# Performance work log

Measured on AMD Instinct MI355X. Metric: run time of the kernel, lower is better.

## Reference

```python
import jax, jax.numpy as jnp
import numpy as np
import math

D_MODEL = 1024
NUM_HEADS = 16
HEAD_DIM = D_MODEL // NUM_HEADS
BLOCK_SIZE = 64
THRESHOLD = 0.99


def setup_inputs() -> dict:
    key = jax.random.key(0)
    ks = jax.random.split(key, 12)
    B, S, D = 2, 2048, D_MODEL
    scale = 1.0 / math.sqrt(D)
    x = jax.random.normal(ks[0], (B, S, D), dtype=jnp.float32)
    G_ii = jax.random.uniform(ks[1], (B, S), dtype=jnp.float32)
    # Linear weights stored as [in, out]; applied as x @ W + b (matches nn.Linear math).
    Wq = jax.random.normal(ks[2], (D, D), dtype=jnp.float32) * scale
    bq = jnp.zeros((D,), dtype=jnp.float32)
    Wk = jax.random.normal(ks[3], (D, D), dtype=jnp.float32) * scale
    bk = jnp.zeros((D,), dtype=jnp.float32)
    Wv = jax.random.normal(ks[4], (D, D), dtype=jnp.float32) * scale
    bv = jnp.zeros((D,), dtype=jnp.float32)
    Wo = jax.random.normal(ks[5], (D, D), dtype=jnp.float32) * scale
    bo = jnp.zeros((D,), dtype=jnp.float32)
    return {"x": x, "G_ii": G_ii, "Wq": Wq, "bq": bq, "Wk": Wk, "bk": bk,
            "Wv": Wv, "bv": bv, "Wo": Wo, "bo": bo}


def reference(x, G_ii, Wq, bq, Wk, bk, Wv, bv, Wo, bo):
    B, S, D = x.shape
    H, hd, bs = NUM_HEADS, HEAD_DIM, BLOCK_SIZE
    nb = S // bs

    # Projections and head split: [B, H, S, hd]
    q = (x @ Wq + bq).reshape(B, S, H, hd).transpose(0, 2, 1, 3)
    k = (x @ Wk + bk).reshape(B, S, H, hd).transpose(0, 2, 1, 3)
    v = (x @ Wv + bv).reshape(B, S, H, hd).transpose(0, 2, 1, 3)

    # Per-query-block scattering energy keep mask: block kept iff max |G_ii| >= threshold
    energy = jnp.abs(G_ii)                              # [B, S]
    block_max = energy.reshape(B, nb, bs).max(axis=-1)  # [B, nb]
    keep = (block_max >= THRESHOLD)                     # [B, nb] bool
    row_keep = jnp.repeat(keep, bs, axis=1)             # [B, S]

    # Kept query blocks attend densely (non-causal) over all keys; skipped blocks output zero.
    scores = jnp.einsum('bhqd,bhkd->bhqk', q, k) / math.sqrt(hd)  # [B, H, S, S]
    attn = jax.nn.softmax(scores, axis=-1)
    out = jnp.einsum('bhqk,bhkd->bhqd', attn, v)                  # [B, H, S, hd]
    out = out * row_keep[:, None, :, None].astype(out.dtype)

    out = out.transpose(0, 2, 1, 3).reshape(B, S, D)
    return out @ Wo + bo
```

## Files before the change

kernel.cpp:

```cpp
#include <hip/hip_runtime.h>
#include <math.h>

#define D_MODEL   1024
#define NUM_HEADS 16
#define HEAD_DIM  64
#define BS        64
#define NB        32
#define S_LEN     2048
#define BATCH     2
#define M_ROWS    (BATCH * S_LEN)
#define THRESH    0.99f
#define SCEXP     0.18033688f
#define NPH       (BATCH * NB * NUM_HEADS)
#define SPLITK    4

typedef __attribute__((ext_vector_type(8))) short bf16x8;
typedef __attribute__((ext_vector_type(8))) _Float16 f16x8;
typedef __attribute__((ext_vector_type(2))) __fp16 fp16v2;
typedef __attribute__((ext_vector_type(4))) float f32x4;

static constexpr size_t QKV_ELEMS = (size_t)BATCH * NUM_HEADS * S_LEN * HEAD_DIM;

__device__ __forceinline__ unsigned short f2bf(float f) {
    unsigned int u = __float_as_uint(f);
    u += 0x7fff + ((u >> 16) & 1);
    return (unsigned short)(u >> 16);
}

__device__ __forceinline__ unsigned int pkrtz(float a, float b) {
    fp16v2 r = __builtin_amdgcn_cvt_pkrtz(a, b);
    return __builtin_bit_cast(unsigned int, r);
}

__device__ __forceinline__ void gload16(const void* gptr, void* lptr) {
    __builtin_amdgcn_global_load_lds(
        (const __attribute__((address_space(1))) void*)gptr,
        (__attribute__((address_space(3))) void*)lptr, 16, 0, 0);
}

__global__ __launch_bounds__(256) void prep_kernel(
    const float* __restrict__ x, const float* __restrict__ G,
    const float* __restrict__ Wq, const float* __restrict__ Wk,
    const float* __restrict__ Wv, const float* __restrict__ Wo,
    unsigned short* __restrict__ xb, unsigned short* __restrict__ wcat,
    unsigned short* __restrict__ wot, int* __restrict__ keep, int* __restrict__ work)
{
    const int bid = blockIdx.x, tid = threadIdx.x;
    __shared__ float T[64][65];

    if (bid < 2048) {
        size_t i = ((size_t)bid * 256 + tid) * 8;
        float4 a = *(const float4*)(x + i);
        float4 b = *(const float4*)(x + i + 4);
        uint4 o;
        o.x = (unsigned int)f2bf(a.x) | ((unsigned int)f2bf(a.y) << 16);
        o.y = (unsigned int)f2bf(a.z) | ((unsigned int)f2bf(a.w) << 16);
        o.z = (unsigned int)f2bf(b.x) | ((unsigned int)f2bf(b.y) << 16);
        o.w = (unsigned int)f2bf(b.z) | ((unsigned int)f2bf(b.w) << 16);
        *(uint4*)(xb + i) = o;
    } else if (bid < 3072) {
        int i = bid - 2048;
        int mat = i >> 8, rem = i & 255;
        int k0 = (rem & 15) * 64, n0 = (rem >> 4) * 64;
        const float* W = (mat == 0) ? Wq : (mat == 1) ? Wk : (mat == 2) ? Wv : Wo;
        int rr = tid >> 4, c4 = (tid & 15) * 4;
        #pragma unroll
        for (int j = 0; j < 4; j++) {
            int row = rr + j * 16;
            float4 v = *(const float4*)(W + (size_t)(k0 + row) * 1024 + n0 + c4);
            T[row][c4 + 0] = v.x; T[row][c4 + 1] = v.y;
            T[row][c4 + 2] = v.z; T[row][c4 + 3] = v.w;
        }
        __syncthreads();
        unsigned short* dst = (mat < 3) ? (wcat + (size_t)mat * 1024 * 1024) : wot;
        #pragma unroll
        for (int j = 0; j < 4; j++) {
            int n = rr + j * 16;
            unsigned int lo = (unsigned int)f2bf(T[c4 + 0][n]) | ((unsigned int)f2bf(T[c4 + 1][n]) << 16);
            unsigned int hi = (unsigned int)f2bf(T[c4 + 2][n]) | ((unsigned int)f2bf(T[c4 + 3][n]) << 16);
            *(uint2*)(dst + (size_t)(n0 + n) * 1024 + k0 + c4) = make_uint2(lo, hi);
        }
    } else {
        if (tid < 64) {
            int t = tid;
            const float4* g = (const float4*)(G + (size_t)t * 64);
            float mx = 0.f;
            #pragma unroll
            for (int j = 0; j < 16; j++) {
                float4 v = g[j];
                mx = fmaxf(mx, fmaxf(fmaxf(fabsf(v.x), fabsf(v.y)), fmaxf(fabsf(v.z), fabsf(v.w))));
            }
            bool k = (mx >= THRESH);
            unsigned long long bal = __ballot(k);
            int nk = __popcll(bal);
            unsigned long long below = bal & ((1ull << t) - 1ull);
            int nbelow = (int)__popcll(below);
            keep[t] = k ? 1 : 0;
            if (t == 0) work[0] = nk;
            int pos = k ? nbelow : (nk + t - nbelow);
            work[1 + pos] = t;
        }
    }
}

__global__ __launch_bounds__(256) void mfma_gemm(
    const unsigned short* __restrict__ A, const unsigned short* __restrict__ Bt,
    const float* __restrict__ b0, const float* __restrict__ b1, const float* __restrict__ b2,
    const int* __restrict__ keep,
    void* __restrict__ out0, unsigned short* __restrict__ out1, unsigned short* __restrict__ out2,
    int mode)
{
    const int K = 1024;
    const int n0 = blockIdx.x * 128, m0 = blockIdx.y * 128;
    const int tid = threadIdx.x, w = tid >> 6, lane = tid & 63;
    const int quad = lane >> 4, l16 = lane & 15;
    const int wm = w >> 1, wn = w & 1;

    const int kb0 = m0 >> 6;
    const bool dropped = (!keep[kb0]) && (!keep[kb0 + 1]);

    if (mode == 1 && (n0 >> 10) == 0 && dropped) return;
    if (mode == 0 && dropped) {
        float* o = (float*)out0;
        #pragma unroll
        for (int i = 0; i < 16; i++) {
            int u = tid + i * 256;
            int row = u >> 5, c = (u & 31) * 4;
            *(float4*)(o + (size_t)(m0 + row) * 1024 + n0 + c) = *(const float4*)(b0 + n0 + c);
        }
        return;
    }

    __shared__ unsigned short Asl[2][128 * 32];
    __shared__ unsigned short Bsl[2][128 * 32];

    f32x4 acc[4][4];
    #pragma unroll
    for (int mt = 0; mt < 4; mt++)
        #pragma unroll
        for (int nt = 0; nt < 4; nt++) acc[mt][nt] = (f32x4){0.f, 0.f, 0.f, 0.f};

    #define GSTAGE(it_, p_)                                                             \
        {                                                                               \
            int k0_ = (it_) * 32;                                                       \
            _Pragma("unroll")                                                           \
            for (int j = 0; j < 2; j++) {                                               \
                int s = w * 128 + j * 64 + lane;                                        \
                int row = s >> 2, cl = s & 3;                                           \
                int c = cl ^ ((row >> 1) & 3);                                          \
                gload16(A  + (size_t)(m0 + row) * K + k0_ + c * 8,                      \
                        &Asl[p_][(size_t)(w * 128 + j * 64) * 8]);                      \
                gload16(Bt + (size_t)(n0 + row) * K + k0_ + c * 8,                      \
                        &Bsl[p_][(size_t)(w * 128 + j * 64) * 8]);                      \
            }                                                                           \
        }

    GSTAGE(0, 0)

    for (int it = 0; it < 32; it++) {
        const int p = it & 1;
        __syncthreads();
        if (it + 1 < 32) GSTAGE(it + 1, (it + 1) & 1)

        bf16x8 af[4], bfr[4];
        #pragma unroll
        for (int mt = 0; mt < 4; mt++) {
            int row = wm * 64 + mt * 16 + l16;
            int cl = quad ^ ((row >> 1) & 3);
            af[mt] = *(const bf16x8*)&Asl[p][(row * 4 + cl) * 8];
        }
        #pragma unroll
        for (int nt = 0; nt < 4; nt++) {
            int row = wn * 64 + nt * 16 + l16;
            int cl = quad ^ ((row >> 1) & 3);
            bfr[nt] = *(const bf16x8*)&Bsl[p][(row * 4 + cl) * 8];
        }
        #pragma unroll
        for (int mt = 0; mt < 4; mt++)
            #pragma unroll
            for (int nt = 0; nt < 4; nt++)
                acc[mt][nt] = __builtin_amdgcn_mfma_f32_16x16x32_bf16(af[mt], bfr[nt], acc[mt][nt], 0, 0, 0);
    }

    if (mode == 0) {
        float* o = (float*)out0;
        #pragma unroll
        for (int nt = 0; nt < 4; nt++) {
            int col = n0 + wn * 64 + nt * 16 + l16;
            float bb = b0[col];
            #pragma unroll
            for (int mt = 0; mt < 4; mt++) {
                int mb = m0 + wm * 64 + mt * 16 + quad * 4;
                #pragma unroll
                for (int r = 0; r < 4; r++)
                    o[(size_t)(mb + r) * 1024 + col] = acc[mt][nt][r] + bb;
            }
        }
    } else {
        #pragma unroll
        for (int nt = 0; nt < 4; nt++) {
            int col = n0 + wn * 64 + nt * 16 + l16;
            int kind = col >> 10, cc = col & 1023;
            int h = cc >> 6, d = cc & 63;
            const float* bp = (kind == 0) ? b0 : (kind == 1) ? b1 : b2;
            float bb = bp[cc];
            #pragma unroll
            for (int mt = 0; mt < 4; mt++) {
                int m = m0 + wm * 64 + mt * 16 + quad * 4;
                int b = m >> 11, s = m & 2047;
                if (kind < 2) {
                    unsigned short* dst = ((kind == 0) ? (unsigned short*)out0 : out1) +
                        ((size_t)(b * NUM_HEADS + h) * S_LEN + s) * HEAD_DIM + d;
                    float sc = (kind == 0) ? SCEXP : 1.0f;
                    #pragma unroll
                    for (int r = 0; r < 4; r++)
                        dst[(size_t)r * HEAD_DIM] = f2bf((acc[mt][nt][r] + bb) * sc);
                } else {
                    unsigned int lo = pkrtz(acc[mt][nt][0] + bb, acc[mt][nt][1] + bb);
                    unsigned int hi = pkrtz(acc[mt][nt][2] + bb, acc[mt][nt][3] + bb);
                    *(uint2*)(out2 + ((size_t)(b * NUM_HEADS + h) * HEAD_DIM + d) * S_LEN + s) =
                        make_uint2(lo, hi);
                }
            }
        }
    }
}

__global__ __launch_bounds__(256, 4) void attn_kernel(
    const unsigned short* __restrict__ Q, const unsigned short* __restrict__ K,
    const unsigned short* __restrict__ Vtg, const int* __restrict__ work,
    unsigned short* __restrict__ opart, float* __restrict__ lpart)
{
    const int bx = blockIdx.x, half = blockIdx.y;
    const int pair = bx >> 4, h = bx & 15;
    const int tid  = threadIdx.x;
    const int w    = tid >> 6, lane = tid & 63;
    const int quad = lane >> 4, l16 = lane & 15;

    if (pair >= work[0]) return;
    const int e = work[1 + pair];
    const int b = e >> 5, qblk = e & 31;

    __shared__ unsigned short Kbuf[BS * HEAD_DIM];
    __shared__ unsigned short Vbuf[HEAD_DIM * BS];
    __shared__ unsigned short Pt[4][16 * 64];

    const int KEYS = S_LEN / SPLITK;
    const int NCH  = KEYS / BS;
    const size_t bh = (size_t)(b * NUM_HEADS + h);
    const unsigned short* Kb = K + bh * S_LEN * HEAD_DIM + (size_t)half * KEYS * HEAD_DIM;
    const unsigned short* Vb = Vtg + bh * HEAD_DIM * S_LEN + (size_t)half * KEYS;
    const unsigned short* Qb = Q + bh * S_LEN * HEAD_DIM;

    const int qrow = qblk * BS + w * 16 + l16;
    bf16x8 qf[2];
    #pragma unroll
    for (int ks = 0; ks < 2; ks++)
        qf[ks] = *(const bf16x8*)(Qb + (size_t)qrow * HEAD_DIM + ks * 32 + quad * 8);

    f32x4 o[4];
    #pragma unroll
    for (int mt = 0; mt < 4; mt++) o[mt] = (f32x4){0.f, 0.f, 0.f, 0.f};
    float l = 0.f;

    const int sA = w * 128 + lane, sB = sA + 64;
    const int rA = sA >> 3, cA = (sA & 7) ^ (rA & 7);
    const int rB = sB >> 3, cB = (sB & 7) ^ (rB & 7);
    const size_t koA = (size_t)rA * HEAD_DIM + cA * 8, koB = (size_t)rB * HEAD_DIM + cB * 8;
    const size_t voA = (size_t)rA * S_LEN + cA * 8,    voB = (size_t)rB * S_LEN + cB * 8;

    uint4 kr0, kr1, vr0, vr1;
    #define LOADREGS(kc_)                                                       \
        {                                                                       \
            const unsigned short* kg_ = Kb + (size_t)(kc_) * BS * HEAD_DIM;     \
            const unsigned short* vg_ = Vb + (size_t)(kc_) * BS;                \
            kr0 = *(const uint4*)(kg_ + koA); kr1 = *(const uint4*)(kg_ + koB); \
            vr0 = *(const uint4*)(vg_ + voA); vr1 = *(const uint4*)(vg_ + voB); \
        }
    #define WRITELDS()                                                          \
        {                                                                       \
            *(uint4*)&Kbuf[(size_t)sA * 8] = kr0;                               \
            *(uint4*)&Kbuf[(size_t)sB * 8] = kr1;                               \
            *(uint4*)&Vbuf[(size_t)sA * 8] = vr0;                               \
            *(uint4*)&Vbuf[(size_t)sB * 8] = vr1;                               \
        }

    LOADREGS(0)
    WRITELDS()
    __syncthreads();

    for (int kc = 0; kc < NCH; kc++) {
        if (kc + 1 < NCH) LOADREGS(kc + 1)

        f32x4 st[4];
        #pragma unroll
        for (int mt = 0; mt < 4; mt++) {
            f32x4 acc = {0.f, 0.f, 0.f, 0.f};
            #pragma unroll
            for (int ks = 0; ks < 2; ks++) {
                int kk = mt * 16 + l16;
                bf16x8 kf = *(const bf16x8*)&Kbuf[(size_t)(kk * 8 + ((ks * 4 + quad) ^ (kk & 7))) * 8];
                acc = __builtin_amdgcn_mfma_f32_16x16x32_bf16(kf, qf[ks], acc, 0, 0, 0);
            }
            st[mt] = acc;
        }

        float pv[16], sum = 0.f;
        #pragma unroll
        for (int mt = 0; mt < 4; mt++)
            #pragma unroll
            for (int r = 0; r < 4; r++) {
                float ex = exp2f(st[mt][r]);
                pv[mt * 4 + r] = ex; sum += ex;
            }
        sum += __shfl_xor(sum, 16, 64);
        sum += __shfl_xor(sum, 32, 64);
        l += sum;

        #pragma unroll
        for (int mt = 0; mt < 4; mt++) {
            unsigned int lo = pkrtz(pv[mt * 4 + 0], pv[mt * 4 + 1]);
            unsigned int hi = pkrtz(pv[mt * 4 + 2], pv[mt * 4 + 3]);
            int c16 = 2 * mt + (quad >> 1);
            *(uint2*)&Pt[w][l16 * 64 + ((c16 ^ (l16 & 7)) * 8 + (quad & 1) * 4)] = make_uint2(lo, hi);
        }

        #pragma unroll
        for (int ks = 0; ks < 2; ks++) {
            f16x8 pf = *(const f16x8*)&Pt[w][l16 * 64 + (((4 * ks + quad) ^ (l16 & 7)) * 8)];
            #pragma unroll
            for (int mt = 0; mt < 4; mt++) {
                int d = mt * 16 + l16;
                f16x8 vf = *(const f16x8*)&Vbuf[(size_t)(d * 8 + ((ks * 4 + quad) ^ (d & 7))) * 8];
                o[mt] = __builtin_amdgcn_mfma_f32_16x16x32_f16(vf, pf, o[mt], 0, 0, 0);
            }
        }

        __syncthreads();
        if (kc + 1 < NCH) {
            WRITELDS()
            __syncthreads();
        }
    }

    unsigned short* ob = opart + ((size_t)(half * NPH + bx)) * 4096 + tid * 16;
    uint4 w0, w1;
    w0.x = pkrtz(o[0][0], o[0][1]); w0.y = pkrtz(o[0][2], o[0][3]);
    w0.z = pkrtz(o[1][0], o[1][1]); w0.w = pkrtz(o[1][2], o[1][3]);
    w1.x = pkrtz(o[2][0], o[2][1]); w1.y = pkrtz(o[2][2], o[2][3]);
    w1.z = pkrtz(o[3][0], o[3][1]); w1.w = pkrtz(o[3][2], o[3][3]);
    *(uint4*)ob = w0;
    *(uint4*)(ob + 8) = w1;
    if (quad == 0) lpart[(size_t)(half * NPH + bx) * 64 + w * 16 + l16] = l;
}

__global__ __launch_bounds__(256) void attn_combine(
    const unsigned short* __restrict__ opart, const float* __restrict__ lpart,
    const int* __restrict__ work, unsigned short* __restrict__ attn_out)
{
    const int bx = blockIdx.x;
    const int pair = bx >> 4, h = bx & 15;
    const int tid  = threadIdx.x;
    const int w    = tid >> 6, lane = tid & 63;
    const int quad = lane >> 4, l16 = lane & 15;

    const int e = work[1 + pair];
    const int b = e >> 5, qblk = e & 31;
    unsigned short* ablk = attn_out + ((size_t)(b * S_LEN + qblk * BS)) * D_MODEL + h * HEAD_DIM;

    if (pair >= work[0]) {
        uint4 z = make_uint4(0, 0, 0, 0);
        #pragma unroll
        for (int i = 0; i < 2; i++) {
            int u = tid + i * 256;
            int row = u >> 3, c8 = (u & 7) * 8;
            *(uint4*)(ablk + (size_t)row * D_MODEL + c8) = z;
        }
        return;
    }

    __shared__ float Obuf[4][HEAD_DIM * 17];

    float osum[16];
    #pragma unroll
    for (int j = 0; j < 16; j++) osum[j] = 0.f;
    float lsum = 0.f;
    #pragma unroll
    for (int hf = 0; hf < SPLITK; hf++) {
        const f16x8* pp = (const f16x8*)(opart + ((size_t)hf * NPH + bx) * 4096 + tid * 16);
        f16x8 a0 = pp[0], a1 = pp[1];
        #pragma unroll
        for (int j = 0; j < 8; j++) {
            osum[j]     += (float)a0[j];
            osum[8 + j] += (float)a1[j];
        }
        lsum += lpart[((size_t)hf * NPH + bx) * 64 + w * 16 + l16];
    }
    float inv = 1.0f / lsum;

    #pragma unroll
    for (int mt = 0; mt < 4; mt++)
        #pragma unroll
        for (int r = 0; r < 4; r++)
            Obuf[w][(mt * 16 + quad * 4 + r) * 17 + l16] = osum[mt * 4 + r] * inv;
    #pragma unroll
    for (int i = 0; i < 4; i++) {
        int uu = lane + 64 * i;
        int row = uu >> 4, d4 = (uu & 15) * 4;
        float x0 = Obuf[w][(d4 + 0) * 17 + row];
        float x1 = Obuf[w][(d4 + 1) * 17 + row];
        float x2 = Obuf[w][(d4 + 2) * 17 + row];
        float x3 = Obuf[w][(d4 + 3) * 17 + row];
        unsigned int lo = (unsigned int)f2bf(x0) | ((unsigned int)f2bf(x1) << 16);
        unsigned int hi = (unsigned int)f2bf(x2) | ((unsigned int)f2bf(x3) << 16);
        *(uint2*)(ablk + (size_t)(w * 16 + row) * D_MODEL + d4) = make_uint2(lo, hi);
    }
}

extern "C" void kernel_launch(void* const* d_in, const int* in_sizes, int n_in,
                              void* d_out, int out_size, void* d_ws, size_t ws_size,
                              hipStream_t stream) {
    const float* x  = (const float*)d_in[0];
    const float* G  = (const float*)d_in[1];
    const float* Wq = (const float*)d_in[2];
    const float* bq = (const float*)d_in[3];
    const float* Wk = (const float*)d_in[4];
    const float* bk = (const float*)d_in[5];
    const float* Wv = (const float*)d_in[6];
    const float* bv = (const float*)d_in[7];
    const float* Wo = (const float*)d_in[8];
    const float* bo = (const float*)d_in[9];
    float* out = (float*)d_out;

    char* wsp = (char*)d_ws;
    int* keep = (int*)wsp;
    int* work = keep + 64;
    unsigned short* xb    = (unsigned short*)(wsp + 1024);
    unsigned short* wcat  = xb + (size_t)M_ROWS * D_MODEL;
    unsigned short* wot   = wcat + (size_t)3 * 1024 * 1024;
    unsigned short* q     = wot + (size_t)1024 * 1024;
    unsigned short* k     = q + QKV_ELEMS;
    unsigned short* vt    = k + QKV_ELEMS;
    unsigned short* attnb = vt + QKV_ELEMS;
    unsigned short* opart = attnb + (size_t)M_ROWS * D_MODEL;
    float* lpart = (float*)(opart + (size_t)SPLITK * NPH * 4096);

    prep_kernel<<<3073, 256, 0, stream>>>(x, G, Wq, Wk, Wv, Wo, xb, wcat, wot, keep, work);

    mfma_gemm<<<dim3(3072 / 128, M_ROWS / 128), 256, 0, stream>>>(
        xb, wcat, bq, bk, bv, keep, (void*)q, k, vt, 1);

    attn_kernel<<<dim3(NPH, SPLITK), 256, 0, stream>>>(q, k, vt, work, opart, lpart);
    attn_combine<<<NPH, 256, 0, stream>>>(opart, lpart, work, attnb);

    mfma_gemm<<<dim3(1024 / 128, M_ROWS / 128), 256, 0, stream>>>(
        attnb, wot, bo, nullptr, nullptr, keep, (void*)out, nullptr, nullptr, 0);
}
```

Baseline: 197.5 us.

## Split GEMM into QKV and output kernels with smaller tiles and coalesced LDS epilogues

Replaces the unified 128x128 GEMM with two specialized kernels. gemm_qkv uses 64x128 tiles, skips Q at single 64-row block granularity, and stages results through LDS to write Q/K row-major into a combined [M,2048] buffer and V transposed with 16-byte stores. gemm_out uses 64x64 tiles with per-block keep skipping. The attention kernel reads Q/K from the new strided layout. Smaller tiles raise the block count and skip granularity but lower per-block data reuse.

```diff
diff --git a/kernel.cpp b/kernel.cpp
--- a/kernel.cpp
+++ b/kernel.cpp
@@ -18,8 +18,6 @@
 typedef __attribute__((ext_vector_type(8))) _Float16 f16x8;
 typedef __attribute__((ext_vector_type(2))) __fp16 fp16v2;
 typedef __attribute__((ext_vector_type(4))) float f32x4;
-
-static constexpr size_t QKV_ELEMS = (size_t)BATCH * NUM_HEADS * S_LEN * HEAD_DIM;
 
 __device__ __forceinline__ unsigned short f2bf(float f) {
     unsigned int u = __float_as_uint(f);
@@ -103,132 +101,205 @@
     }
 }
 
-__global__ __launch_bounds__(256) void mfma_gemm(
+__global__ __launch_bounds__(256, 4) void gemm_qkv(
     const unsigned short* __restrict__ A, const unsigned short* __restrict__ Bt,
-    const float* __restrict__ b0, const float* __restrict__ b1, const float* __restrict__ b2,
-    const int* __restrict__ keep,
-    void* __restrict__ out0, unsigned short* __restrict__ out1, unsigned short* __restrict__ out2,
-    int mode)
+    const float* __restrict__ bq, const float* __restrict__ bk, const float* __restrict__ bv,
+    const int* __restrict__ keep, unsigned short* __restrict__ qk, unsigned short* __restrict__ vt)
 {
-    const int K = 1024;
-    const int n0 = blockIdx.x * 128, m0 = blockIdx.y * 128;
+    const int n0 = blockIdx.x * 128, m0 = blockIdx.y * 64;
+    const int tid = threadIdx.x, w = tid >> 6, lane = tid & 63;
+    const int quad = lane >> 4, l16 = lane & 15;
+    const int kindb = n0 >> 10;
+    if (kindb == 0 && !keep[blockIdx.y]) return;
+
+    __shared__ union {
+        struct { unsigned short As[2][64 * 32]; unsigned short Bs[2][128 * 32]; } s;
+        unsigned short qkr[64 * 136];
+        unsigned short vr[128 * 72];
+    } u;
+
+    f32x4 acc[4][2];
+    #pragma unroll
+    for (int mt = 0; mt < 4; mt++)
+        #pragma unroll
+        for (int nt = 0; nt < 2; nt++) acc[mt][nt] = (f32x4){0.f, 0.f, 0.f, 0.f};
+
+    #define QSTAGE(it_, p_)                                                             \
+        {                                                                               \
+            int k0_ = (it_) * 32;                                                       \
+            { int s_ = w * 64 + lane; int row = s_ >> 2, cl = s_ & 3;                   \
+              int c = cl ^ ((row >> 1) & 3);                                            \
+              gload16(A + (size_t)(m0 + row) * 1024 + k0_ + c * 8,                      \
+                      &u.s.As[p_][(w * 64) * 8]); }                                     \
+            _Pragma("unroll")                                                           \
+            for (int j = 0; j < 2; j++) {                                               \
+                int s_ = w * 128 + j * 64 + lane; int row = s_ >> 2, cl = s_ & 3;       \
+                int c = cl ^ ((row >> 1) & 3);                                          \
+                gload16(Bt + (size_t)(n0 + row) * 1024 + k0_ + c * 8,                   \
+                        &u.s.Bs[p_][(w * 128 + j * 64) * 8]);                           \
+            }                                                                           \
+        }
+
+    QSTAGE(0, 0)
+
+    for (int it = 0; it < 32; it++) {
+        const int p = it & 1;
+        __syncthreads();
+        if (it + 1 < 32) QSTAGE(it + 1, (it + 1) & 1)
+
+        bf16x8 af[4], bfr[2];
+        #pragma unroll
+        for (int mt = 0; mt < 4; mt++) {
+            int row = mt * 16 + l16;
+            int cl = quad ^ ((row >> 1) & 3);
+            af[mt] = *(const bf16x8*)&u.s.As[p][(row * 4 + cl) * 8];
+        }
+        #pragma unroll
+        for (int nt = 0; nt < 2; nt++) {
+            int row = w * 32 + nt * 16 + l16;
+            int cl = quad ^ ((row >> 1) & 3);
+            bfr[nt] = *(const bf16x8*)&u.s.Bs[p][(row * 4 + cl) * 8];
+        }
+        #pragma unroll
+        for (int mt = 0; mt < 4; mt++)
+            #pragma unroll
+            for (int nt = 0; nt < 2; nt++)
+                acc[mt][nt] = __builtin_amdgcn_mfma_f32_16x16x32_bf16(af[mt], bfr[nt], acc[mt][nt], 0, 0, 0);
+    }
+    __syncthreads();
+
+    if (kindb < 2) {
+        const float* bp = (kindb == 0) ? bq : bk;
+        const float sc = (kindb == 0) ? SCEXP : 1.0f;
+        #pragma unroll
+        for (int nt = 0; nt < 2; nt++) {
+            int coll = w * 32 + nt * 16 + l16;
+            float bb = bp[(n0 & 1023) + coll];
+            #pragma unroll
+            for (int mt = 0; mt < 4; mt++)
+                #pragma unroll
+                for (int r = 0; r < 4; r++) {
+                    int row = mt * 16 + quad * 4 + r;
+                    u.qkr[row * 136 + coll] = f2bf((acc[mt][nt][r] + bb) * sc);
+                }
+        }
+        __syncthreads();
+        #pragma unroll
+        for (int i = 0; i < 4; i++) {
+            int s_ = tid + i * 256;
+            int row = s_ >> 4, c16 = s_ & 15;
+            uint4 v = *(const uint4*)&u.qkr[row * 136 + c16 * 8];
+            *(uint4*)(qk + (size_t)(m0 + row) * 2048 + n0 + c16 * 8) = v;
+        }
+    } else {
+        #pragma unroll
+        for (int nt = 0; nt < 2; nt++) {
+            int coll = w * 32 + nt * 16 + l16;
+            float bb = bv[(n0 - 2048) + coll];
+            #pragma unroll
+            for (int mt = 0; mt < 4; mt++) {
+                int s0 = mt * 16 + quad * 4;
+                uint2 pv;
+                pv.x = pkrtz(acc[mt][nt][0] + bb, acc[mt][nt][1] + bb);
+                pv.y = pkrtz(acc[mt][nt][2] + bb, acc[mt][nt][3] + bb);
+                *(uint2*)&u.vr[coll * 72 + s0] = pv;
+            }
+        }
+        __syncthreads();
+        const int b_ = m0 >> 11, sbase = m0 & 2047;
+        #pragma unroll
+        for (int i = 0; i < 4; i++) {
+            int s_ = tid + i * 256;
+            int coll = s_ >> 3, ch = s_ & 7;
+            uint4 v = *(const uint4*)&u.vr[coll * 72 + ch * 8];
+            int colg = n0 - 2048 + coll;
+            int h_ = colg >> 6, d = colg & 63;
+            *(uint4*)(vt + ((size_t)(b_ * NUM_HEADS + h_) * HEAD_DIM + d) * 2048 + sbase + ch * 8) = v;
+        }
+    }
+}
+
+__global__ __launch_bounds__(256, 4) void gemm_out(
+    const unsigned short* __restrict__ A, const unsigned short* __restrict__ Bt,
+    const float* __restrict__ bo, const int* __restrict__ keep, float* __restrict__ out)
+{
+    const int n0 = blockIdx.x * 64, m0 = blockIdx.y * 64;
     const int tid = threadIdx.x, w = tid >> 6, lane = tid & 63;
     const int quad = lane >> 4, l16 = lane & 15;
     const int wm = w >> 1, wn = w & 1;
 
-    const int kb0 = m0 >> 6;
-    const bool dropped = (!keep[kb0]) && (!keep[kb0 + 1]);
-
-    if (mode == 1 && (n0 >> 10) == 0 && dropped) return;
-    if (mode == 0 && dropped) {
-        float* o = (float*)out0;
-        #pragma unroll
-        for (int i = 0; i < 16; i++) {
-            int u = tid + i * 256;
-            int row = u >> 5, c = (u & 31) * 4;
-            *(float4*)(o + (size_t)(m0 + row) * 1024 + n0 + c) = *(const float4*)(b0 + n0 + c);
+    if (!keep[blockIdx.y]) {
+        #pragma unroll
+        for (int i = 0; i < 4; i++) {
+            int s_ = tid + i * 256;
+            int row = s_ >> 4, c = (s_ & 15) * 4;
+            *(float4*)(out + (size_t)(m0 + row) * 1024 + n0 + c) = *(const float4*)(bo + n0 + c);
         }
         return;
     }
 
-    __shared__ unsigned short Asl[2][128 * 32];
-    __shared__ unsigned short Bsl[2][128 * 32];
-
-    f32x4 acc[4][4];
-    #pragma unroll
-    for (int mt = 0; mt < 4; mt++)
-        #pragma unroll
-        for (int nt = 0; nt < 4; nt++) acc[mt][nt] = (f32x4){0.f, 0.f, 0.f, 0.f};
-
-    #define GSTAGE(it_, p_)                                                             \
+    __shared__ unsigned short Asl[2][64 * 32];
+    __shared__ unsigned short Bsl[2][64 * 32];
+
+    f32x4 acc[2][2];
+    #pragma unroll
+    for (int mt = 0; mt < 2; mt++)
+        #pragma unroll
+        for (int nt = 0; nt < 2; nt++) acc[mt][nt] = (f32x4){0.f, 0.f, 0.f, 0.f};
+
+    #define OSTAGE(it_, p_)                                                             \
         {                                                                               \
             int k0_ = (it_) * 32;                                                       \
-            _Pragma("unroll")                                                           \
-            for (int j = 0; j < 2; j++) {                                               \
-                int s = w * 128 + j * 64 + lane;                                        \
-                int row = s >> 2, cl = s & 3;                                           \
-                int c = cl ^ ((row >> 1) & 3);                                          \
-                gload16(A  + (size_t)(m0 + row) * K + k0_ + c * 8,                      \
-                        &Asl[p_][(size_t)(w * 128 + j * 64) * 8]);                      \
-                gload16(Bt + (size_t)(n0 + row) * K + k0_ + c * 8,                      \
-                        &Bsl[p_][(size_t)(w * 128 + j * 64) * 8]);                      \
-            }                                                                           \
-        }
-
-    GSTAGE(0, 0)
+            int s_ = w * 64 + lane; int row = s_ >> 2, cl = s_ & 3;                     \
+            int c = cl ^ ((row >> 1) & 3);                                              \
+            gload16(A  + (size_t)(m0 + row) * 1024 + k0_ + c * 8, &Asl[p_][(w * 64) * 8]); \
+            gload16(Bt + (size_t)(n0 + row) * 1024 + k0_ + c * 8, &Bsl[p_][(w * 64) * 8]); \
+        }
+
+    OSTAGE(0, 0)
 
     for (int it = 0; it < 32; it++) {
         const int p = it & 1;
         __syncthreads();
-        if (it + 1 < 32) GSTAGE(it + 1, (it + 1) & 1)
-
-        bf16x8 af[4], bfr[4];
-        #pragma unroll
-        for (int mt = 0; mt < 4; mt++) {
-            int row = wm * 64 + mt * 16 + l16;
+        if (it + 1 < 32) OSTAGE(it + 1, (it + 1) & 1)
+
+        bf16x8 af[2], bfr[2];
+        #pragma unroll
+        for (int mt = 0; mt < 2; mt++) {
+            int row = wm * 32 + mt * 16 + l16;
             int cl = quad ^ ((row >> 1) & 3);
             af[mt] = *(const bf16x8*)&Asl[p][(row * 4 + cl) * 8];
         }
         #pragma unroll
-        for (int nt = 0; nt < 4; nt++) {
-            int row = wn * 64 + nt * 16 + l16;
+        for (int nt = 0; nt < 2; nt++) {
+            int row = wn * 32 + nt * 16 + l16;
             int cl = quad ^ ((row >> 1) & 3);
             bfr[nt] = *(const bf16x8*)&Bsl[p][(row * 4 + cl) * 8];
         }
         #pragma unroll
-        for (int mt = 0; mt < 4; mt++)
-            #pragma unroll
-            for (int nt = 0; nt < 4; nt++)
+        for (int mt = 0; mt < 2; mt++)
+            #pragma unroll
+            for (int nt = 0; nt < 2; nt++)
                 acc[mt][nt] = __builtin_amdgcn_mfma_f32_16x16x32_bf16(af[mt], bfr[nt], acc[mt][nt], 0, 0, 0);
     }
 
-    if (mode == 0) {
-        float* o = (float*)out0;
-        #pragma unroll
-        for (int nt = 0; nt < 4; nt++) {
-            int col = n0 + wn * 64 + nt * 16 + l16;
-            float bb = b0[col];
-            #pragma unroll
-            for (int mt = 0; mt < 4; mt++) {
-                int mb = m0 + wm * 64 + mt * 16 + quad * 4;
-                #pragma unroll
-                for (int r = 0; r < 4; r++)
-                    o[(size_t)(mb + r) * 1024 + col] = acc[mt][nt][r] + bb;
-            }
-        }
-    } else {
-        #pragma unroll
-        for (int nt = 0; nt < 4; nt++) {
-            int col = n0 + wn * 64 + nt * 16 + l16;
-            int kind = col >> 10, cc = col & 1023;
-            int h = cc >> 6, d = cc & 63;
-            const float* bp = (kind == 0) ? b0 : (kind == 1) ? b1 : b2;
-            float bb = bp[cc];
-            #pragma unroll
-            for (int mt = 0; mt < 4; mt++) {
-                int m = m0 + wm * 64 + mt * 16 + quad * 4;
-                int b = m >> 11, s = m & 2047;
-                if (kind < 2) {
-                    unsigned short* dst = ((kind == 0) ? (unsigned short*)out0 : out1) +
-                        ((size_t)(b * NUM_HEADS + h) * S_LEN + s) * HEAD_DIM + d;
-                    float sc = (kind == 0) ? SCEXP : 1.0f;
-                    #pragma unroll
-                    for (int r = 0; r < 4; r++)
-                        dst[(size_t)r * HEAD_DIM] = f2bf((acc[mt][nt][r] + bb) * sc);
-                } else {
-                    unsigned int lo = pkrtz(acc[mt][nt][0] + bb, acc[mt][nt][1] + bb);
-                    unsigned int hi = pkrtz(acc[mt][nt][2] + bb, acc[mt][nt][3] + bb);
-                    *(uint2*)(out2 + ((size_t)(b * NUM_HEADS + h) * HEAD_DIM + d) * S_LEN + s) =
-                        make_uint2(lo, hi);
-                }
-            }
+    #pragma unroll
+    for (int nt = 0; nt < 2; nt++) {
+        int col = n0 + wn * 32 + nt * 16 + l16;
+        float bb = bo[col];
+        #pragma unroll
+        for (int mt = 0; mt < 2; mt++) {
+            int mb = m0 + wm * 32 + mt * 16 + quad * 4;
+            #pragma unroll
+            for (int r = 0; r < 4; r++)
+                out[(size_t)(mb + r) * 1024 + col] = acc[mt][nt][r] + bb;
         }
     }
 }
 
 __global__ __launch_bounds__(256, 4) void attn_kernel(
-    const unsigned short* __restrict__ Q, const unsigned short* __restrict__ K,
-    const unsigned short* __restrict__ Vtg, const int* __restrict__ work,
+    const unsigned short* __restrict__ qk, const unsigned short* __restrict__ Vtg,
+    const int* __restrict__ work,
     unsigned short* __restrict__ opart, float* __restrict__ lpart)
 {
     const int bx = blockIdx.x, half = blockIdx.y;
@@ -247,16 +318,15 @@
 
     const int KEYS = S_LEN / SPLITK;
     const int NCH  = KEYS / BS;
-    const size_t bh = (size_t)(b * NUM_HEADS + h);
-    const unsigned short* Kb = K + bh * S_LEN * HEAD_DIM + (size_t)half * KEYS * HEAD_DIM;
-    const unsigned short* Vb = Vtg + bh * HEAD_DIM * S_LEN + (size_t)half * KEYS;
-    const unsigned short* Qb = Q + bh * S_LEN * HEAD_DIM;
+    const unsigned short* Qb = qk + (size_t)(b * S_LEN) * 2048 + h * 64;
+    const unsigned short* Kb = qk + (size_t)(b * S_LEN + half * KEYS) * 2048 + 1024 + h * 64;
+    const unsigned short* Vb = Vtg + (size_t)(b * NUM_HEADS + h) * HEAD_DIM * 2048 + half * KEYS;
 
     const int qrow = qblk * BS + w * 16 + l16;
     bf16x8 qf[2];
     #pragma unroll
     for (int ks = 0; ks < 2; ks++)
-        qf[ks] = *(const bf16x8*)(Qb + (size_t)qrow * HEAD_DIM + ks * 32 + quad * 8);
+        qf[ks] = *(const bf16x8*)(Qb + (size_t)qrow * 2048 + ks * 32 + quad * 8);
 
     f32x4 o[4];
     #pragma unroll
@@ -266,16 +336,15 @@
     const int sA = w * 128 + lane, sB = sA + 64;
     const int rA = sA >> 3, cA = (sA & 7) ^ (rA & 7);
     const int rB = sB >> 3, cB = (sB & 7) ^ (rB & 7);
-    const size_t koA = (size_t)rA * HEAD_DIM + cA * 8, koB = (size_t)rB * HEAD_DIM + cB * 8;
-    const size_t voA = (size_t)rA * S_LEN + cA * 8,    voB = (size_t)rB * S_LEN + cB * 8;
+    const size_t koA = (size_t)rA * 2048 + cA * 8, koB = (size_t)rB * 2048 + cB * 8;
 
     uint4 kr0, kr1, vr0, vr1;
     #define LOADREGS(kc_)                                                       \
         {                                                                       \
-            const unsigned short* kg_ = Kb + (size_t)(kc_) * BS * HEAD_DIM;     \
+            const unsigned short* kg_ = Kb + (size_t)(kc_) * BS * 2048;         \
             const unsigned short* vg_ = Vb + (size_t)(kc_) * BS;                \
             kr0 = *(const uint4*)(kg_ + koA); kr1 = *(const uint4*)(kg_ + koB); \
-            vr0 = *(const uint4*)(vg_ + voA); vr1 = *(const uint4*)(vg_ + voB); \
+            vr0 = *(const uint4*)(vg_ + koA); vr1 = *(const uint4*)(vg_ + koB); \
         }
     #define WRITELDS()                                                          \
         {                                                                       \
@@ -438,21 +507,19 @@
     unsigned short* xb    = (unsigned short*)(wsp + 1024);
     unsigned short* wcat  = xb + (size_t)M_ROWS * D_MODEL;
     unsigned short* wot   = wcat + (size_t)3 * 1024 * 1024;
-    unsigned short* q     = wot + (size_t)1024 * 1024;
-    unsigned short* k     = q + QKV_ELEMS;
-    unsigned short* vt    = k + QKV_ELEMS;
-    unsigned short* attnb = vt + QKV_ELEMS;
+    unsigned short* qk    = wot + (size_t)1024 * 1024;
+    unsigned short* vt    = qk + (size_t)M_ROWS * 2048;
+    unsigned short* attnb = vt + (size_t)BATCH * NUM_HEADS * HEAD_DIM * 2048;
     unsigned short* opart = attnb + (size_t)M_ROWS * D_MODEL;
     float* lpart = (float*)(opart + (size_t)SPLITK * NPH * 4096);
 
     prep_kernel<<<3073, 256, 0, stream>>>(x, G, Wq, Wk, Wv, Wo, xb, wcat, wot, keep, work);
 
-    mfma_gemm<<<dim3(3072 / 128, M_ROWS / 128), 256, 0, stream>>>(
-        xb, wcat, bq, bk, bv, keep, (void*)q, k, vt, 1);
-
-    attn_kernel<<<dim3(NPH, SPLITK), 256, 0, stream>>>(q, k, vt, work, opart, lpart);
+    gemm_qkv<<<dim3(3072 / 128, M_ROWS / 64), 256, 0, stream>>>(
+        xb, wcat, bq, bk, bv, keep, qk, vt);
+
+    attn_kernel<<<dim3(NPH, SPLITK), 256, 0, stream>>>(qk, vt, work, opart, lpart);
     attn_combine<<<NPH, 256, 0, stream>>>(opart, lpart, work, attnb);
 
-    mfma_gemm<<<dim3(1024 / 128, M_ROWS / 128), 256, 0, stream>>>(
-        attnb, wot, bo, nullptr, nullptr, keep, (void*)out, nullptr, nullptr, 0);
-}
+    gemm_out<<<dim3(1024 / 64, M_ROWS / 64), 256, 0, stream>>>(attnb, wot, bo, keep, out);
+}
```

Measured after the change: 191.8 us. -2.9%, faster.
